# Kernel tuning notes

Hardware: AMD Instinct MI355X
Metric: run time of the kernel (lower is better)

## Reference

```python
import jax, jax.numpy as jnp
import numpy as np

B, N, C, H = 2, 2048, 512, 8
D = C // H
SCALE = D ** (-0.5)


def setup_inputs() -> dict:
    key = jax.random.key(0)
    k1, k2, k3 = jax.random.split(key, 3)
    x = jax.random.normal(k1, (B, N, C), dtype=jnp.float32)
    qkv_w = jax.random.normal(k2, (C, 3 * C), dtype=jnp.float32) * (C ** -0.5)
    proj_w = jax.random.normal(k3, (C, C), dtype=jnp.float32) * (C ** -0.5)
    proj_b = jnp.zeros((C,), dtype=jnp.float32)
    return {"x": x, "qkv_w": qkv_w, "proj_w": proj_w, "proj_b": proj_b}


def reference(x, qkv_w, proj_w, proj_b):
    # qkv projection (no bias) -> (B, N, 3, H, D) -> (3, B, H, N, D)
    qkv = jnp.einsum('bnc,cf->bnf', x, qkv_w)
    qkv = qkv.reshape(B, N, 3, H, D).transpose(2, 0, 3, 1, 4)
    q, k, v = qkv[0], qkv[1], qkv[2]
    q = q * SCALE
    attn = jnp.einsum('bhid,bhjd->bhij', q, k)          # (B, H, N, N)
    attn = jax.nn.softmax(attn, axis=-1)
    out = jnp.einsum('bhij,bhjd->bhid', attn, v)         # (B, H, N, D)
    # Faithful to source: reshape (B,H,N,D) -> (B,N,C) WITHOUT transposing
    out = out.reshape(B, N, C)
    out = jnp.einsum('bnc,cd->bnd', out, proj_w) + proj_b
    return out
```

## Files before the change

kernel.cpp:

```cpp
#include <hip/hip_runtime.h>
#include <math.h>

constexpr int Bb = 2;
constexpr int Nn = 2048;
constexpr int Cc = 512;
constexpr int Hh = 8;
constexpr int Dd = 64;

typedef short short8 __attribute__((ext_vector_type(8)));
typedef float floatx4 __attribute__((ext_vector_type(4)));
typedef float floatx16 __attribute__((ext_vector_type(16)));

__device__ inline short8 bcs8(uint4 u) { return __builtin_bit_cast(short8, u); }

__device__ inline floatx4 mfma16(short8 a, short8 b, floatx4 c) {
    return __builtin_amdgcn_mfma_f32_16x16x32_bf16(a, b, c, 0, 0, 0);
}
__device__ inline floatx16 mfma32(short8 a, short8 b, floatx16 c) {
    return __builtin_amdgcn_mfma_f32_32x32x16_bf16(a, b, c, 0, 0, 0);
}

#if __has_builtin(__builtin_amdgcn_exp2f)
#define EXP2(x) __builtin_amdgcn_exp2f(x)
#else
#define EXP2(x) __expf((x) * 0.69314718056f)
#endif

__device__ inline unsigned pk_trunc(float a, float b) {
    return __builtin_amdgcn_perm(__float_as_uint(b), __float_as_uint(a), 0x07060302u);
}
__device__ inline unsigned pk_rne(float a, float b) {
    unsigned ua = __float_as_uint(a); ua += 0x7fffu + ((ua >> 16) & 1u);
    unsigned ub = __float_as_uint(b); ub += 0x7fffu + ((ub >> 16) & 1u);
    return __builtin_amdgcn_perm(ub, ua, 0x07060302u);
}
__device__ inline unsigned short rne1(float a) {
    unsigned u = __float_as_uint(a); u += 0x7fffu + ((u >> 16) & 1u);
    return (unsigned short)(u >> 16);
}
__device__ inline float tr16(float a) {
    return __uint_as_float(__float_as_uint(a) & 0xffff0000u);
}
__device__ inline void split8(float4 A, float4 B, uint4& hi, uint4& lo) {
    hi = make_uint4(pk_trunc(A.x, A.y), pk_trunc(A.z, A.w),
                    pk_trunc(B.x, B.y), pk_trunc(B.z, B.w));
    lo = make_uint4(pk_trunc(A.x - tr16(A.x), A.y - tr16(A.y)),
                    pk_trunc(A.z - tr16(A.z), A.w - tr16(A.w)),
                    pk_trunc(B.x - tr16(B.x), B.y - tr16(B.y)),
                    pk_trunc(B.z - tr16(B.z), B.w - tr16(B.w)));
}


__global__ __launch_bounds__(256) void prep(const float* __restrict__ qkv_w,
                                            const float* __restrict__ proj_w,
                                            const float* __restrict__ x,
                                            unsigned short* __restrict__ wqfrag,
                                            unsigned short* __restrict__ wpfrag,
                                            unsigned short* __restrict__ xfrag)
{
    int bid = blockIdx.x;
    int t = threadIdx.x;
    if (bid >= 256) {
        int mt = bid - 256;
        const float* xs = x + (size_t)mt * 16 * 512;
        unsigned short* slab = xfrag + (size_t)mt * 16384;
        #pragma unroll
        for (int i = 0; i < 4; ++i) {
            int q = i * 256 + t;
            int kc = q >> 6, f = q & 63;
            int m = f & 15, o = f >> 4;
            const float* p = xs + m * 512 + kc * 32 + o * 8;
            float4 A = *(const float4*)p;
            float4 B = *(const float4*)(p + 4);
            uint4 hi, lo; split8(A, B, hi, lo);
            unsigned short* d = slab + kc * 1024 + f * 8;
            *(uint4*)d = hi;
            *(uint4*)(d + 512) = lo;
        }
        return;
    }
    const float* src; unsigned short* dfrag; int W, f0, k0;
    if (bid < 192) { int kt = bid / 24, ft = bid % 24; W = 1536; src = qkv_w; dfrag = wqfrag; f0 = ft * 64; k0 = kt * 64; }
    else { int b2 = bid - 192; int kt = b2 / 8, ft = b2 % 8; W = 512; src = proj_w; dfrag = wpfrag; f0 = ft * 64; k0 = kt * 64; }
    #pragma unroll
    for (int i = 0; i < 2; ++i) {
        int s = i * 256 + t;
        int fp = s >> 6, l = s & 63;
        int nt = fp >> 1, kc = fp & 1;
        int m = l & 15, o = l >> 4;
        int f = f0 + nt * 16 + m;
        int kbase = k0 + kc * 32 + o * 8;
        float F[8];
        #pragma unroll
        for (int j = 0; j < 8; ++j) F[j] = src[(size_t)(kbase + j) * W + f];
        uint4 hi, lo;
        split8(make_float4(F[0], F[1], F[2], F[3]),
               make_float4(F[4], F[5], F[6], F[7]), hi, lo);
        int ntg = (f0 >> 4) + nt, kcg = (k0 >> 5) + kc;
        unsigned short* d = dfrag + ((size_t)(ntg * 16 + kcg) * 2) * 512 + l * 8;
        *(uint4*)d = hi;
        *(uint4*)(d + 512) = lo;
    }
}

__global__ __launch_bounds__(256, 3) void gemm_qkv(const unsigned short* __restrict__ xfrag,
                                                   const unsigned short* __restrict__ wqfrag,
                                                   unsigned short* __restrict__ qd,
                                                   unsigned short* __restrict__ kfrag,
                                                   unsigned short* __restrict__ vfrag)
{
    const int tid = threadIdx.x, lane = tid & 63, w = tid >> 6;
    const int l15 = lane & 15, l4 = lane >> 4;
    const int row0 = blockIdx.y * 64, col0 = blockIdx.x * 128;
    const int mt0 = row0 >> 4;
    const int nt0 = (col0 >> 4) + w * 2;

    floatx4 acc[4][2];
    #pragma unroll
    for (int i = 0; i < 4; ++i)
        #pragma unroll
        for (int j = 0; j < 2; ++j)
            #pragma unroll
            for (int r = 0; r < 4; ++r) acc[i][j][r] = 0.f;

    const unsigned short* xb = xfrag + (size_t)lane * 8;
    const unsigned short* wb = wqfrag + (size_t)lane * 8;

    #pragma unroll
    for (int kc = 0; kc < 16; ++kc) {
        short8 bf[2][2];
        #pragma unroll
        for (int nt = 0; nt < 2; ++nt) {
            size_t fb_ = ((size_t)((nt0 + nt) * 16 + kc) * 2) * 512;
            bf[nt][0] = bcs8(*(const uint4*)(wb + fb_));
            bf[nt][1] = bcs8(*(const uint4*)(wb + fb_ + 512));
        }
        #pragma unroll
        for (int mt = 0; mt < 4; ++mt) {
            size_t fa_ = ((size_t)((mt0 + mt) * 16 + kc) * 2) * 512;
            short8 ah = bcs8(*(const uint4*)(xb + fa_));
            short8 al = bcs8(*(const uint4*)(xb + fa_ + 512));
            #pragma unroll
            for (int nt = 0; nt < 2; ++nt) {
                acc[mt][nt] = mfma16(ah, bf[nt][0], acc[mt][nt]);
                acc[mt][nt] = mfma16(ah, bf[nt][1], acc[mt][nt]);
                acc[mt][nt] = mfma16(al, bf[nt][0], acc[mt][nt]);
            }
        }
    }
    #pragma unroll
    for (int mt = 0; mt < 4; ++mt)
        #pragma unroll
        for (int nt = 0; nt < 2; ++nt) {
            int c = col0 + (w * 2 + nt) * 16 + l15;
            int which = c >> 9;
            int head = (c >> 6) & 7, d = c & 63;
            int tokb = row0 + mt * 16 + l4 * 4;
            int b = tokb >> 11, nn = tokb & 2047;
            int bh = b * 8 + head;
            if (which == 0) {
                #pragma unroll
                for (int r = 0; r < 4; ++r)
                    qd[(size_t)(bh * 2048 + nn + r) * 64 + d] = rne1(acc[mt][nt][r] * 0.18033688f);
            } else if (which == 1) {
                int s = d >> 4;
                size_t fb_ = ((size_t)(bh * 64 + (nn >> 5)) * 4 + s) * 512 + (d & 7);
                int hl = ((d >> 3) & 1) * 32;
                #pragma unroll
                for (int r = 0; r < 4; ++r)
                    kfrag[fb_ + (size_t)(hl + ((nn + r) & 31)) * 8] = rne1(acc[mt][nt][r]);
            } else {
                int j = nn >> 4, mtv = d >> 5;
                uint2 pv;
                pv.x = pk_rne(acc[mt][nt][0], acc[mt][nt][1]);
                pv.y = pk_rne(acc[mt][nt][2], acc[mt][nt][3]);
                *(uint2*)&vfrag[((size_t)(bh * 128 + j) * 2 + mtv) * 512 +
                                (size_t)(((nn >> 3) & 1) * 32 + (d & 31)) * 8 + (nn & 7)] = pv;
            }
        }
}

__global__ __launch_bounds__(256, 2) void attn(const unsigned short* __restrict__ qd,
                                               const unsigned short* __restrict__ kfrag,
                                               const unsigned short* __restrict__ vfrag,
                                               unsigned short* __restrict__ Ofrag)
{
    __shared__ float Pp[2][64][65];
    __shared__ float Lsp[2][64];

    int bid = blockIdx.x;
    int xcd = bid & 7; int rr = bid >> 3;
    int qt = rr & 31; int bhi = rr >> 5;
    int bh = (bhi << 3) | xcd;
    int tid = threadIdx.x, lane = tid & 63, kg = tid >> 6;
    int l31 = lane & 31, h = lane >> 5;

    short8 qf[2][4];
    #pragma unroll
    for (int qh = 0; qh < 2; ++qh)
        #pragma unroll
        for (int s = 0; s < 4; ++s)
            qf[qh][s] = bcs8(*(const uint4*)(qd + ((size_t)bh * 2048 + qt * 64 + qh * 32 + l31) * 64 + s * 16 + h * 8));

    const uint4 onesu = make_uint4(0x3F803F80u, 0x3F803F80u, 0x3F803F80u, 0x3F803F80u);
    const short8 onesf = bcs8(onesu);

    floatx16 OT[2][2], OTl[2];
    #pragma unroll
    for (int qh = 0; qh < 2; ++qh) {
        #pragma unroll
        for (int i = 0; i < 2; ++i)
            #pragma unroll
            for (int r = 0; r < 16; ++r) OT[qh][i][r] = 0.f;
        #pragma unroll
        for (int r = 0; r < 16; ++r) OTl[qh][r] = 0.f;
    }

    const unsigned short* kb_ = kfrag + ((size_t)(bh * 64 + kg * 16) * 4) * 512 + lane * 8;
    const unsigned short* vb_ = vfrag + ((size_t)(bh * 128 + kg * 32) * 2) * 512 + lane * 8;

    #pragma unroll
    for (int c = 0; c < 16; ++c) {
        uint4 kfu[4];
        #pragma unroll
        for (int s = 0; s < 4; ++s)
            kfu[s] = *(const uint4*)(kb_ + ((size_t)c * 4 + s) * 512);
        uint4 vfu[2][2];
        #pragma unroll
        for (int kc = 0; kc < 2; ++kc)
            #pragma unroll
            for (int mtv = 0; mtv < 2; ++mtv)
                vfu[kc][mtv] = *(const uint4*)(vb_ + ((size_t)(c * 2 + kc) * 2 + mtv) * 512);

        #pragma unroll
        for (int qh = 0; qh < 2; ++qh) {
            floatx16 st;
            #pragma unroll
            for (int r = 0; r < 16; ++r) st[r] = 0.f;
            #pragma unroll
            for (int s = 0; s < 4; ++s) st = mfma32(bcs8(kfu[s]), qf[qh][s], st);

            unsigned P2[8];
            #pragma unroll
            for (int s2 = 0; s2 < 8; ++s2)
                P2[s2] = pk_trunc(EXP2(st[2 * s2]), EXP2(st[2 * s2 + 1]));

            #pragma unroll
            for (int kc = 0; kc < 2; ++kc) {
                unsigned X0 = P2[4 * kc + 0], X1 = P2[4 * kc + 1];
                unsigned Y0 = P2[4 * kc + 2], Y1 = P2[4 * kc + 3];
                unsigned T0 = h ? X0 : Y0;
                unsigned T1 = h ? X1 : Y1;
                unsigned To0 = __shfl_xor(T0, 32, 64);
                unsigned To1 = __shfl_xor(T1, 32, 64);
                uint4 fu;
                fu.x = h ? To0 : X0;
                fu.y = h ? To1 : X1;
                fu.z = h ? Y0 : To0;
                fu.w = h ? Y1 : To1;
                short8 pf = bcs8(fu);
                OT[qh][0] = mfma32(bcs8(vfu[kc][0]), pf, OT[qh][0]);
                OT[qh][1] = mfma32(bcs8(vfu[kc][1]), pf, OT[qh][1]);
                OTl[qh] = mfma32(onesf, pf, OTl[qh]);
            }
        }
    }

    if (kg < 2) {
        #pragma unroll
        for (int qh = 0; qh < 2; ++qh) {
            int q = qh * 32 + l31;
            #pragma unroll
            for (int mtv = 0; mtv < 2; ++mtv)
                #pragma unroll
                for (int r = 0; r < 16; ++r) {
                    int d = mtv * 32 + (r & 3) + 8 * (r >> 2) + 4 * h;
                    Pp[kg][q][d] = OT[qh][mtv][r];
                }
            Lsp[kg][q] = OTl[qh][0];
        }
    }
    __syncthreads();
    if (kg >= 2) {
        #pragma unroll
        for (int qh = 0; qh < 2; ++qh) {
            int q = qh * 32 + l31;
            #pragma unroll
            for (int mtv = 0; mtv < 2; ++mtv)
                #pragma unroll
                for (int r = 0; r < 16; ++r) {
                    int d = mtv * 32 + (r & 3) + 8 * (r >> 2) + 4 * h;
                    Pp[kg - 2][q][d] += OT[qh][mtv][r];
                }
            if (h == 0) Lsp[kg - 2][q] += OTl[qh][0];
        }
    }
    __syncthreads();
    {
        int q = tid >> 2, dc = (tid & 3) * 16;
        float linv = 1.f / (Lsp[0][q] + Lsp[1][q]);
        float vv[16];
        #pragma unroll
        for (int i = 0; i < 16; ++i)
            vv[i] = (Pp[0][q][dc + i] + Pp[1][q][dc + i]) * linv;
        unsigned hi[8], lo[8];
        #pragma unroll
        for (int i = 0; i < 8; ++i) {
            float a = vv[2 * i], bb = vv[2 * i + 1];
            hi[i] = pk_trunc(a, bb);
            lo[i] = pk_trunc(a - tr16(a), bb - tr16(bb));
        }
        int ng = qt * 64 + q;
        int r = bh * 256 + (ng >> 3);
        int mt = r >> 4, m = r & 15;
        #pragma unroll
        for (int hh = 0; hh < 2; ++hh) {
            int cc = (ng & 7) * 64 + dc + hh * 8;
            int kc = cc >> 5, oct = (cc >> 3) & 3;
            unsigned short* fb_ = Ofrag + ((size_t)(mt * 16 + kc) * 2) * 512 + (m + 16 * oct) * 8;
            *(uint4*)fb_ = make_uint4(hi[4 * hh + 0], hi[4 * hh + 1], hi[4 * hh + 2], hi[4 * hh + 3]);
            *(uint4*)(fb_ + 512) = make_uint4(lo[4 * hh + 0], lo[4 * hh + 1], lo[4 * hh + 2], lo[4 * hh + 3]);
        }
    }
}

__global__ __launch_bounds__(256, 2) void gemm_proj(const unsigned short* __restrict__ Ofrag,
                                                    const unsigned short* __restrict__ wpfrag,
                                                    const float* __restrict__ bias,
                                                    float* __restrict__ out)
{
    const int tid = threadIdx.x, lane = tid & 63, w = tid >> 6;
    const int l15 = lane & 15, l4 = lane >> 4;
    const int row0 = blockIdx.y * 64, col0 = blockIdx.x * 64;
    const int wm = w >> 1, wn = w & 1;
    const int mt0 = (row0 >> 4) + wm * 2;
    const int nt0 = (col0 >> 4) + wn * 2;

    floatx4 acc[2][2];
    #pragma unroll
    for (int i = 0; i < 2; ++i)
        #pragma unroll
        for (int j = 0; j < 2; ++j)
            #pragma unroll
            for (int r = 0; r < 4; ++r) acc[i][j][r] = 0.f;

    const unsigned short* ab = Ofrag + (size_t)lane * 8;
    const unsigned short* wb = wpfrag + (size_t)lane * 8;

    #pragma unroll
    for (int kc = 0; kc < 16; ++kc) {
        short8 bf[2][2];
        #pragma unroll
        for (int nt = 0; nt < 2; ++nt) {
            size_t fb_ = ((size_t)((nt0 + nt) * 16 + kc) * 2) * 512;
            bf[nt][0] = bcs8(*(const uint4*)(wb + fb_));
            bf[nt][1] = bcs8(*(const uint4*)(wb + fb_ + 512));
        }
        #pragma unroll
        for (int mt = 0; mt < 2; ++mt) {
            size_t fa_ = ((size_t)((mt0 + mt) * 16 + kc) * 2) * 512;
            short8 ah = bcs8(*(const uint4*)(ab + fa_));
            short8 al = bcs8(*(const uint4*)(ab + fa_ + 512));
            #pragma unroll
            for (int nt = 0; nt < 2; ++nt) {
                acc[mt][nt] = mfma16(ah, bf[nt][0], acc[mt][nt]);
                acc[mt][nt] = mfma16(ah, bf[nt][1], acc[mt][nt]);
                acc[mt][nt] = mfma16(al, bf[nt][0], acc[mt][nt]);
            }
        }
    }
    #pragma unroll
    for (int mt = 0; mt < 2; ++mt)
        #pragma unroll
        for (int nt = 0; nt < 2; ++nt) {
            int c = col0 + wn * 32 + nt * 16 + l15;
            float bv = bias[c];
            #pragma unroll
            for (int r = 0; r < 4; ++r) {
                int tok = row0 + wm * 32 + mt * 16 + l4 * 4 + r;
                out[(size_t)tok * 512 + c] = acc[mt][nt][r] + bv;
            }
        }
}

extern "C" void kernel_launch(void* const* d_in, const int* in_sizes, int n_in,
                              void* d_out, int out_size, void* d_ws, size_t ws_size,
                              hipStream_t stream)
{
    const float* x      = (const float*)d_in[0];
    const float* qkv_w  = (const float*)d_in[1];
    const float* proj_w = (const float*)d_in[2];
    const float* proj_b = (const float*)d_in[3];
    float* out = (float*)d_out;

    char* ws = (char*)d_ws;
    unsigned short* xfrag  = (unsigned short*)ws;
    unsigned short* wqfrag = (unsigned short*)(ws + 8388608);
    unsigned short* wpfrag = (unsigned short*)(ws + 11534336);
    unsigned short* qd     = (unsigned short*)(ws + 12582912);
    unsigned short* kfrag  = (unsigned short*)(ws + 16777216);
    unsigned short* vfrag  = (unsigned short*)(ws + 20971520);
    unsigned short* Ofrag  = (unsigned short*)(ws + 25165824);

    prep<<<512, 256, 0, stream>>>(qkv_w, proj_w, x, wqfrag, wpfrag, xfrag);
    gemm_qkv<<<dim3(12, 64), 256, 0, stream>>>(xfrag, wqfrag, qd, kfrag, vfrag);
    attn<<<512, 256, 0, stream>>>(qd, kfrag, vfrag, Ofrag);
    gemm_proj<<<dim3(8, 64), 256, 0, stream>>>(Ofrag, wpfrag, proj_b, out);
}
```

Baseline: 136.1 us.

## Split K dimension across doubled waves in GEMM and attention kernels

Each of the three main kernels now launches 512 threads per block instead of 256. Each half (or quarter, in attention) of the waves processes a slice of the reduction or key dimension, and partial results are combined through shared memory. The goal is more waves in flight to hide memory latency and shorter per-wave serial loops, since the grids are small relative to the CU count. The cost is extra LDS traffic, a block-wide barrier, idle waves during the final reduction, and higher register and LDS pressure under the new launch bounds.

```diff
diff --git a/kernel.cpp b/kernel.cpp
--- a/kernel.cpp
+++ b/kernel.cpp
@@ -103,17 +103,19 @@
     }
 }
 
-__global__ __launch_bounds__(256, 3) void gemm_qkv(const unsigned short* __restrict__ xfrag,
+__global__ __launch_bounds__(512, 4) void gemm_qkv(const unsigned short* __restrict__ xfrag,
                                                    const unsigned short* __restrict__ wqfrag,
                                                    unsigned short* __restrict__ qd,
                                                    unsigned short* __restrict__ kfrag,
                                                    unsigned short* __restrict__ vfrag)
 {
+    __shared__ float Am[4][64][33];
     const int tid = threadIdx.x, lane = tid & 63, w = tid >> 6;
+    const int wq = w & 3, kh = w >> 2;
     const int l15 = lane & 15, l4 = lane >> 4;
     const int row0 = blockIdx.y * 64, col0 = blockIdx.x * 128;
     const int mt0 = row0 >> 4;
-    const int nt0 = (col0 >> 4) + w * 2;
+    const int nt0 = (col0 >> 4) + wq * 2;
 
     floatx4 acc[4][2];
     #pragma unroll
@@ -127,7 +129,8 @@
     const unsigned short* wb = wqfrag + (size_t)lane * 8;
 
     #pragma unroll
-    for (int kc = 0; kc < 16; ++kc) {
+    for (int kk = 0; kk < 8; ++kk) {
+        int kc = kh * 8 + kk;
         short8 bf[2][2];
         #pragma unroll
         for (int nt = 0; nt < 2; ++nt) {
@@ -148,11 +151,30 @@
             }
         }
     }
+    if (kh == 1) {
+        #pragma unroll
+        for (int mt = 0; mt < 4; ++mt)
+            #pragma unroll
+            for (int nt = 0; nt < 2; ++nt)
+                #pragma unroll
+                for (int r = 0; r < 4; ++r)
+                    Am[wq][lane][(mt * 2 + nt) * 4 + r] = acc[mt][nt][r];
+    }
+    __syncthreads();
+    if (kh == 1) return;
     #pragma unroll
     for (int mt = 0; mt < 4; ++mt)
         #pragma unroll
+        for (int nt = 0; nt < 2; ++nt)
+            #pragma unroll
+            for (int r = 0; r < 4; ++r)
+                acc[mt][nt][r] += Am[wq][lane][(mt * 2 + nt) * 4 + r];
+
+    #pragma unroll
+    for (int mt = 0; mt < 4; ++mt)
+        #pragma unroll
         for (int nt = 0; nt < 2; ++nt) {
-            int c = col0 + (w * 2 + nt) * 16 + l15;
+            int c = col0 + (wq * 2 + nt) * 16 + l15;
             int which = c >> 9;
             int head = (c >> 6) & 7, d = c & 63;
             int tokb = row0 + mt * 16 + l4 * 4;
@@ -180,13 +202,13 @@
         }
 }
 
-__global__ __launch_bounds__(256, 2) void attn(const unsigned short* __restrict__ qd,
+__global__ __launch_bounds__(512, 4) void attn(const unsigned short* __restrict__ qd,
                                                const unsigned short* __restrict__ kfrag,
                                                const unsigned short* __restrict__ vfrag,
                                                unsigned short* __restrict__ Ofrag)
 {
-    __shared__ float Pp[2][64][65];
-    __shared__ float Lsp[2][64];
+    __shared__ float Pp[4][64][65];
+    __shared__ float Lsp[4][64];
 
     int bid = blockIdx.x;
     int xcd = bid & 7; int rr = bid >> 3;
@@ -216,11 +238,11 @@
         for (int r = 0; r < 16; ++r) OTl[qh][r] = 0.f;
     }
 
-    const unsigned short* kb_ = kfrag + ((size_t)(bh * 64 + kg * 16) * 4) * 512 + lane * 8;
-    const unsigned short* vb_ = vfrag + ((size_t)(bh * 128 + kg * 32) * 2) * 512 + lane * 8;
-
-    #pragma unroll
-    for (int c = 0; c < 16; ++c) {
+    const unsigned short* kb_ = kfrag + ((size_t)(bh * 64 + kg * 8) * 4) * 512 + lane * 8;
+    const unsigned short* vb_ = vfrag + ((size_t)(bh * 128 + kg * 16) * 2) * 512 + lane * 8;
+
+    #pragma unroll
+    for (int c = 0; c < 8; ++c) {
         uint4 kfu[4];
         #pragma unroll
         for (int s = 0; s < 4; ++s)
@@ -266,7 +288,7 @@
         }
     }
 
-    if (kg < 2) {
+    if (kg < 4) {
         #pragma unroll
         for (int qh = 0; qh < 2; ++qh) {
             int q = qh * 32 + l31;
@@ -281,7 +303,7 @@
         }
     }
     __syncthreads();
-    if (kg >= 2) {
+    if (kg >= 4) {
         #pragma unroll
         for (int qh = 0; qh < 2; ++qh) {
             int q = qh * 32 + l31;
@@ -290,22 +312,23 @@
                 #pragma unroll
                 for (int r = 0; r < 16; ++r) {
                     int d = mtv * 32 + (r & 3) + 8 * (r >> 2) + 4 * h;
-                    Pp[kg - 2][q][d] += OT[qh][mtv][r];
+                    Pp[kg - 4][q][d] += OT[qh][mtv][r];
                 }
-            if (h == 0) Lsp[kg - 2][q] += OTl[qh][0];
+            if (h == 0) Lsp[kg - 4][q] += OTl[qh][0];
         }
     }
     __syncthreads();
     {
-        int q = tid >> 2, dc = (tid & 3) * 16;
-        float linv = 1.f / (Lsp[0][q] + Lsp[1][q]);
-        float vv[16];
-        #pragma unroll
-        for (int i = 0; i < 16; ++i)
-            vv[i] = (Pp[0][q][dc + i] + Pp[1][q][dc + i]) * linv;
-        unsigned hi[8], lo[8];
-        #pragma unroll
-        for (int i = 0; i < 8; ++i) {
+        int q = tid >> 3, dc = (tid & 7) * 8;
+        float linv = 1.f / (Lsp[0][q] + Lsp[1][q] + Lsp[2][q] + Lsp[3][q]);
+        float vv[8];
+        #pragma unroll
+        for (int i = 0; i < 8; ++i)
+            vv[i] = (Pp[0][q][dc + i] + Pp[1][q][dc + i] +
+                     Pp[2][q][dc + i] + Pp[3][q][dc + i]) * linv;
+        unsigned hi[4], lo[4];
+        #pragma unroll
+        for (int i = 0; i < 4; ++i) {
             float a = vv[2 * i], bb = vv[2 * i + 1];
             hi[i] = pk_trunc(a, bb);
             lo[i] = pk_trunc(a - tr16(a), bb - tr16(bb));
@@ -313,26 +336,25 @@
         int ng = qt * 64 + q;
         int r = bh * 256 + (ng >> 3);
         int mt = r >> 4, m = r & 15;
-        #pragma unroll
-        for (int hh = 0; hh < 2; ++hh) {
-            int cc = (ng & 7) * 64 + dc + hh * 8;
-            int kc = cc >> 5, oct = (cc >> 3) & 3;
-            unsigned short* fb_ = Ofrag + ((size_t)(mt * 16 + kc) * 2) * 512 + (m + 16 * oct) * 8;
-            *(uint4*)fb_ = make_uint4(hi[4 * hh + 0], hi[4 * hh + 1], hi[4 * hh + 2], hi[4 * hh + 3]);
-            *(uint4*)(fb_ + 512) = make_uint4(lo[4 * hh + 0], lo[4 * hh + 1], lo[4 * hh + 2], lo[4 * hh + 3]);
-        }
-    }
-}
-
-__global__ __launch_bounds__(256, 2) void gemm_proj(const unsigned short* __restrict__ Ofrag,
+        int cc = (ng & 7) * 64 + dc;
+        int kc = cc >> 5, oct = (cc >> 3) & 3;
+        unsigned short* fb_ = Ofrag + ((size_t)(mt * 16 + kc) * 2) * 512 + (m + 16 * oct) * 8;
+        *(uint4*)fb_ = make_uint4(hi[0], hi[1], hi[2], hi[3]);
+        *(uint4*)(fb_ + 512) = make_uint4(lo[0], lo[1], lo[2], lo[3]);
+    }
+}
+
+__global__ __launch_bounds__(512, 4) void gemm_proj(const unsigned short* __restrict__ Ofrag,
                                                     const unsigned short* __restrict__ wpfrag,
                                                     const float* __restrict__ bias,
                                                     float* __restrict__ out)
 {
+    __shared__ float Am[4][64][17];
     const int tid = threadIdx.x, lane = tid & 63, w = tid >> 6;
+    const int wq = w & 3, kh = w >> 2;
     const int l15 = lane & 15, l4 = lane >> 4;
     const int row0 = blockIdx.y * 64, col0 = blockIdx.x * 64;
-    const int wm = w >> 1, wn = w & 1;
+    const int wm = wq >> 1, wn = wq & 1;
     const int mt0 = (row0 >> 4) + wm * 2;
     const int nt0 = (col0 >> 4) + wn * 2;
 
@@ -348,7 +370,8 @@
     const unsigned short* wb = wpfrag + (size_t)lane * 8;
 
     #pragma unroll
-    for (int kc = 0; kc < 16; ++kc) {
+    for (int kk = 0; kk < 8; ++kk) {
+        int kc = kh * 8 + kk;
         short8 bf[2][2];
         #pragma unroll
         for (int nt = 0; nt < 2; ++nt) {
@@ -369,6 +392,17 @@
             }
         }
     }
+    if (kh == 1) {
+        #pragma unroll
+        for (int mt = 0; mt < 2; ++mt)
+            #pragma unroll
+            for (int nt = 0; nt < 2; ++nt)
+                #pragma unroll
+                for (int r = 0; r < 4; ++r)
+                    Am[wq][lane][(mt * 2 + nt) * 4 + r] = acc[mt][nt][r];
+    }
+    __syncthreads();
+    if (kh == 1) return;
     #pragma unroll
     for (int mt = 0; mt < 2; ++mt)
         #pragma unroll
@@ -378,7 +412,8 @@
             #pragma unroll
             for (int r = 0; r < 4; ++r) {
                 int tok = row0 + wm * 32 + mt * 16 + l4 * 4 + r;
-                out[(size_t)tok * 512 + c] = acc[mt][nt][r] + bv;
+                out[(size_t)tok * 512 + c] =
+                    acc[mt][nt][r] + Am[wq][lane][(mt * 2 + nt) * 4 + r] + bv;
             }
         }
 }
@@ -403,7 +438,7 @@
     unsigned short* Ofrag  = (unsigned short*)(ws + 25165824);
 
     prep<<<512, 256, 0, stream>>>(qkv_w, proj_w, x, wqfrag, wpfrag, xfrag);
-    gemm_qkv<<<dim3(12, 64), 256, 0, stream>>>(xfrag, wqfrag, qd, kfrag, vfrag);
-    attn<<<512, 256, 0, stream>>>(qd, kfrag, vfrag, Ofrag);
-    gemm_proj<<<dim3(8, 64), 256, 0, stream>>>(Ofrag, wpfrag, proj_b, out);
-}
+    gemm_qkv<<<dim3(12, 64), 512, 0, stream>>>(xfrag, wqfrag, qd, kfrag, vfrag);
+    attn<<<512, 512, 0, stream>>>(qd, kfrag, vfrag, Ofrag);
+    gemm_proj<<<dim3(8, 64), 512, 0, stream>>>(Ofrag, wpfrag, proj_b, out);
+}
```

Result: slower. 330.7 us (+143.0%).

## Stage QKV GEMM A-fragments through double-buffered LDS with register prefetch

Applied to the files above, without the earlier changes.

In the QKV projection kernel, the four wavefronts now load the shared x fragments into a double-buffered LDS tile cooperatively, instead of each wave reading the same A fragments from global memory. The next k-chunk is prefetched into registers while MFMAs run on the current buffer. This cuts redundant global and L2 traffic for A, at the cost of two barriers per k-step, 16KB of LDS, and dropping full unrolling of the k loop.

```diff
diff --git a/kernel.cpp b/kernel.cpp
--- a/kernel.cpp
+++ b/kernel.cpp
@@ -109,6 +109,7 @@
                                                    unsigned short* __restrict__ kfrag,
                                                    unsigned short* __restrict__ vfrag)
 {
+    __shared__ unsigned short Abuf[2][4096];
     const int tid = threadIdx.x, lane = tid & 63, w = tid >> 6;
     const int l15 = lane & 15, l4 = lane >> 4;
     const int row0 = blockIdx.y * 64, col0 = blockIdx.x * 128;
@@ -123,11 +124,37 @@
             #pragma unroll
             for (int r = 0; r < 4; ++r) acc[i][j][r] = 0.f;
 
-    const unsigned short* xb = xfrag + (size_t)lane * 8;
     const unsigned short* wb = wqfrag + (size_t)lane * 8;
 
-    #pragma unroll
+    uint4 vst[2];
+    {
+        #pragma unroll
+        for (int i = 0; i < 2; ++i) {
+            int c = i * 256 + tid;
+            int f = c >> 6, j = c & 63;
+            const unsigned short* s = xfrag +
+                ((size_t)((mt0 + (f >> 1)) * 16 + 0) * 2 + (f & 1)) * 512 + j * 8;
+            vst[i] = *(const uint4*)s;
+        }
+        #pragma unroll
+        for (int i = 0; i < 2; ++i)
+            *(uint4*)(Abuf[0] + (i * 256 + tid) * 8) = vst[i];
+    }
+
+    int cur = 0;
     for (int kc = 0; kc < 16; ++kc) {
+        __syncthreads();
+        uint4 vnx[2];
+        if (kc < 15) {
+            #pragma unroll
+            for (int i = 0; i < 2; ++i) {
+                int c = i * 256 + tid;
+                int f = c >> 6, j = c & 63;
+                const unsigned short* s = xfrag +
+                    ((size_t)((mt0 + (f >> 1)) * 16 + (kc + 1)) * 2 + (f & 1)) * 512 + j * 8;
+                vnx[i] = *(const uint4*)s;
+            }
+        }
         short8 bf[2][2];
         #pragma unroll
         for (int nt = 0; nt < 2; ++nt) {
@@ -135,11 +162,11 @@
             bf[nt][0] = bcs8(*(const uint4*)(wb + fb_));
             bf[nt][1] = bcs8(*(const uint4*)(wb + fb_ + 512));
         }
+        const unsigned short* Ac = Abuf[cur];
         #pragma unroll
         for (int mt = 0; mt < 4; ++mt) {
-            size_t fa_ = ((size_t)((mt0 + mt) * 16 + kc) * 2) * 512;
-            short8 ah = bcs8(*(const uint4*)(xb + fa_));
-            short8 al = bcs8(*(const uint4*)(xb + fa_ + 512));
+            short8 ah = bcs8(*(const uint4*)(Ac + (mt * 2 + 0) * 512 + lane * 8));
+            short8 al = bcs8(*(const uint4*)(Ac + (mt * 2 + 1) * 512 + lane * 8));
             #pragma unroll
             for (int nt = 0; nt < 2; ++nt) {
                 acc[mt][nt] = mfma16(ah, bf[nt][0], acc[mt][nt]);
@@ -147,7 +174,15 @@
                 acc[mt][nt] = mfma16(al, bf[nt][0], acc[mt][nt]);
             }
         }
-    }
+        __syncthreads();
+        if (kc < 15) {
+            #pragma unroll
+            for (int i = 0; i < 2; ++i)
+                *(uint4*)(Abuf[cur ^ 1] + (i * 256 + tid) * 8) = vnx[i];
+        }
+        cur ^= 1;
+    }
+
     #pragma unroll
     for (int mt = 0; mt < 4; ++mt)
         #pragma unroll
```

After: 148.3 us. 1.09x slower.
